# Kernel optimization log

Measured on AMD Instinct MI355X. Metric: run time of the kernel, lower is better.

The kernel has to match this reference:

```python
import jax, jax.numpy as jnp
import numpy as np

# dims
B, SL, RATIO = 2, 2048, 16
SG = SL // RATIO            # 128 global tokens
S = SL + SG                 # 2176 combined sequence
V, D, H, F, L, NC = 32000, 512, 8, 2048, 2, 8
HD = D // H
PAD = 0


def setup_inputs() -> dict:
    key = jax.random.key(0)
    ks = iter(jax.random.split(key, 40))
    def n(shape, s=0.02):
        return jax.random.normal(next(ks), shape, dtype=jnp.float32) * s
    token_ids = jax.random.randint(next(ks), (B, SL), 0, V)
    embed_table = n((V, D), 1.0).at[PAD].set(0.0)  # padding_idx row is zero
    return {
        "token_ids": token_ids,
        "embed_table": embed_table,
        "global_embed": n((D,), 1.0),              # shared learned global token
        "in_proj_w": n((L, 3 * D, D)), "in_proj_b": jnp.zeros((L, 3 * D)),
        "out_w": n((L, D, D)), "out_b": jnp.zeros((L, D)),
        "ln1_g": jnp.ones((L, D)), "ln1_b": jnp.zeros((L, D)),
        "ln2_g": jnp.ones((L, D)), "ln2_b": jnp.zeros((L, D)),
        "ff1_w": n((L, F, D)), "ff1_b": jnp.zeros((L, F)),
        "ff2_w": n((L, D, F)), "ff2_b": jnp.zeros((L, D)),
        "cls_w1": n((D // 2, D)), "cls_w2": n((NC, D // 2)),
    }


def _layernorm(x, g, b, eps=1e-5):
    mu = x.mean(-1, keepdims=True)
    var = ((x - mu) ** 2).mean(-1, keepdims=True)
    return (x - mu) * jax.lax.rsqrt(var + eps) * g + b


def _etc_bias(pad_long, pad_glob):
    # structured local/global mask: l2l block-diagonal by segment, l2g/g2l
    # long<->its own global token, g2g full. All four components enabled.
    seg = jnp.repeat(jnp.arange(SG), RATIO)          # (SL,) segment id per long token
    gid = jnp.arange(SG)
    l2l = seg[:, None] == seg[None, :]               # (SL, SL)
    l2g = seg[:, None] == gid[None, :]               # (SL, SG)
    allowed = jnp.block([[l2l, l2g],
                         [l2g.T, jnp.ones((SG, SG), bool)]])  # (S, S)
    kpad = jnp.concatenate([pad_long, pad_glob], axis=1)       # (B, S)
    ok = allowed[None] & (~kpad)[:, None, :]
    return jnp.where(ok, 0.0, -1e9)[:, None]          # (B, 1, S, S)


def reference(token_ids, embed_table, global_embed, in_proj_w, in_proj_b,
              out_w, out_b, ln1_g, ln1_b, ln2_g, ln2_b,
              ff1_w, ff1_b, ff2_w, ff2_b, cls_w1, cls_w2):
    pad_long = token_ids == PAD                      # (B, SL)
    pad_glob = pad_long.reshape(B, SG, RATIO).all(-1)  # (B, SG)
    x_long = embed_table[token_ids]                  # (B, SL, D)
    x_glob = jnp.broadcast_to(global_embed, (B, SG, D))
    x = jnp.concatenate([x_long, x_glob], axis=1)    # (B, S, D)
    bias = _etc_bias(pad_long, pad_glob)
    scale = 1.0 / np.sqrt(HD)
    for i in range(L):  # post-norm TransformerEncoderLayer, relu FFN, dropout=0
        qkv = x @ in_proj_w[i].T + in_proj_b[i]
        q, k, v = jnp.split(qkv, 3, axis=-1)
        q = q.reshape(B, S, H, HD)
        k = k.reshape(B, S, H, HD)
        v = v.reshape(B, S, H, HD)
        att = jnp.einsum('bqhd,bkhd->bhqk', q, k) * scale + bias
        att = jax.nn.softmax(att, axis=-1)
        o = jnp.einsum('bhqk,bkhd->bqhd', att, v).reshape(B, S, D)
        x = _layernorm(x + o @ out_w[i].T + out_b[i], ln1_g[i], ln1_b[i])
        h = jax.nn.relu(x @ ff1_w[i].T + ff1_b[i])
        x = _layernorm(x + h @ ff2_w[i].T + ff2_b[i], ln2_g[i], ln2_b[i])
    # masked mean-pool over global tokens
    zg = jnp.where(pad_glob[..., None], 0.0, x[:, SL:, :])
    denom = (~pad_glob).sum(axis=1, keepdims=True).astype(zg.dtype)
    z_cls = zg.sum(axis=1) / denom                   # (B, D)
    return jax.nn.relu(z_cls @ cls_w1.T) @ cls_w2.T  # (B, NC)
```

## Files before the change

### kernel.cpp

```cpp
#include <hip/hip_runtime.h>
#include <hip/hip_bf16.h>
#include <stdint.h>


namespace {

constexpr int kB  = 2;
constexpr int kSL = 2048;
constexpr int kSG = 128;
constexpr int kS  = 2176;
constexpr int kD  = 512;
constexpr int kH  = 8;
constexpr int kF  = 2048;
constexpr int kNC = 8;
constexpr int kM  = kB * kS;

typedef __bf16 bf16x8 __attribute__((ext_vector_type(8)));
typedef unsigned short u16x8 __attribute__((ext_vector_type(8)));
typedef float  f32x4  __attribute__((ext_vector_type(4)));
using bf16 = __hip_bfloat16;

__device__ __forceinline__ void gload16(const void* g, void* l) {
  __builtin_amdgcn_global_load_lds(
      (const __attribute__((address_space(1))) void*)g,
      (__attribute__((address_space(3))) void*)l, 16, 0, 0);
}

__device__ __forceinline__ float bfu2f(unsigned short u) {
  return __uint_as_float(((unsigned int)u) << 16);
}

__device__ __forceinline__ int xcd_swz(int i, int T) {
  return (i & 7) * (T >> 3) + (i >> 3);
}

__global__ __launch_bounds__(256) void cvt4_kernel(
    const float* __restrict__ s0, bf16* __restrict__ d0,
    const float* __restrict__ s1, bf16* __restrict__ d1,
    const float* __restrict__ s2, bf16* __restrict__ d2,
    const float* __restrict__ s3, bf16* __restrict__ d3) {
  constexpr int n0 = 2 * 1536 * 512 / 4;
  constexpr int n1 = 2 * 512 * 512 / 4;
  constexpr int n2 = 2 * 2048 * 512 / 4;
  constexpr int n3 = 2 * 512 * 2048 / 4;
  constexpr int total = n0 + n1 + n2 + n3;
  for (int i = blockIdx.x * 256 + threadIdx.x; i < total;
       i += gridDim.x * 256) {
    const float* src;
    bf16* dst;
    int j = i;
    if (j < n0) { src = s0; dst = d0; }
    else if ((j -= n0) < n1) { src = s1; dst = d1; }
    else if ((j -= n1) < n2) { src = s2; dst = d2; }
    else { j -= n2; src = s3; dst = d3; }
    float4 v = ((const float4*)src)[j];
    dst[j * 4 + 0] = __float2bfloat16(v.x);
    dst[j * 4 + 1] = __float2bfloat16(v.y);
    dst[j * 4 + 2] = __float2bfloat16(v.z);
    dst[j * 4 + 3] = __float2bfloat16(v.w);
  }
}

__global__ __launch_bounds__(128) void embed_kernel(
    const int* __restrict__ tok, const float* __restrict__ table,
    const float* __restrict__ gemb, float* __restrict__ x,
    bf16* __restrict__ x_bf, unsigned char* __restrict__ pad_long,
    unsigned char* __restrict__ pad_glob) {
  const int row = blockIdx.x;
  const int t = threadIdx.x;
  if (row == kM) {
    for (int i = t; i < kB * kSG; i += 128) {
      const int b = i >> 7, g = i & 127;
      bool all = true;
      for (int j = 0; j < 16; ++j)
        all = all && (tok[b * kSL + g * 16 + j] == 0);
      pad_glob[i] = all ? 1 : 0;
    }
    return;
  }
  const int b = row / kS, s = row % kS;
  const float* src;
  if (s < kSL) {
    const int tk = tok[b * kSL + s];
    if (t == 0) pad_long[b * kSL + s] = (tk == 0) ? 1 : 0;
    src = table + (size_t)tk * kD;
  } else {
    src = gemb;
  }
  float4 v = *(const float4*)(src + t * 4);
  *(float4*)(x + (size_t)row * kD + t * 4) = v;
  bf16* xb = x_bf + (size_t)row * kD + t * 4;
  xb[0] = __float2bfloat16(v.x);
  xb[1] = __float2bfloat16(v.y);
  xb[2] = __float2bfloat16(v.z);
  xb[3] = __float2bfloat16(v.w);
}

template <int OUT_MODE>
__global__ __launch_bounds__(256) void gemm_bt(
    const bf16* __restrict__ A, const bf16* __restrict__ W,
    const float* __restrict__ bias, void* __restrict__ Cout,
    int M, int N, int K) {
  __shared__ __align__(16) bf16 As[128 * 32];
  __shared__ __align__(16) bf16 Bs[128 * 32];
  const int t = threadIdx.x;
  const int lane = t & 63;
  const int wid = t >> 6;
  const int wm = wid >> 1, wn = wid & 1;
  const int NB = N >> 7;
  const int swz = xcd_swz(blockIdx.x, gridDim.x);
  const int bm = (swz / NB) * 128, bn = (swz % NB) * 128;
  const int srow = t >> 2, scol = (t & 3) * 8;

  f32x4 acc[4][4];
#pragma unroll
  for (int mi = 0; mi < 4; ++mi)
#pragma unroll
    for (int ni = 0; ni < 4; ++ni)
#pragma unroll
      for (int r = 0; r < 4; ++r) acc[mi][ni][r] = 0.f;

  const bf16* a0 = A + (size_t)(bm + srow) * K + scol;
  const bf16* a1 = a0 + (size_t)64 * K;
  const bf16* w0 = W + (size_t)(bn + srow) * K + scol;
  const bf16* w1p = w0 + (size_t)64 * K;

  for (int k0 = 0; k0 < K; k0 += 32) {
    gload16(a0 + k0, &As[t * 8]);
    gload16(a1 + k0, &As[2048 + t * 8]);
    gload16(w0 + k0, &Bs[t * 8]);
    gload16(w1p + k0, &Bs[2048 + t * 8]);
    __syncthreads();
    bf16x8 af[4], wf[4];
#pragma unroll
    for (int mi = 0; mi < 4; ++mi)
      af[mi] = *(const bf16x8*)&As[(wm * 64 + mi * 16 + (lane & 15)) * 32 +
                                   (lane >> 4) * 8];
#pragma unroll
    for (int ni = 0; ni < 4; ++ni)
      wf[ni] = *(const bf16x8*)&Bs[(wn * 64 + ni * 16 + (lane & 15)) * 32 +
                                   (lane >> 4) * 8];
#pragma unroll
    for (int mi = 0; mi < 4; ++mi)
#pragma unroll
      for (int ni = 0; ni < 4; ++ni)
        acc[mi][ni] = __builtin_amdgcn_mfma_f32_16x16x32_bf16(
            af[mi], wf[ni], acc[mi][ni], 0, 0, 0);
    __syncthreads();
  }

  const int lr = (lane >> 4) * 4;
  const int lc = lane & 15;
#pragma unroll
  for (int ni = 0; ni < 4; ++ni) {
    const int col = bn + wn * 64 + ni * 16 + lc;
    const float bv = bias[col];
#pragma unroll
    for (int mi = 0; mi < 4; ++mi) {
#pragma unroll
      for (int r = 0; r < 4; ++r) {
        const int row = bm + wm * 64 + mi * 16 + lr + r;
        float v = acc[mi][ni][r] + bv;
        if (OUT_MODE == 2) v = fmaxf(v, 0.f);
        ((bf16*)Cout)[(size_t)row * N + col] = __float2bfloat16(v);
      }
    }
  }
}

__global__ __launch_bounds__(256) void gemm_res(
    const bf16* __restrict__ A, const bf16* __restrict__ W,
    const float* __restrict__ bias, float* __restrict__ X, int K) {
  __shared__ __align__(16) bf16 As[64 * 32];
  __shared__ __align__(16) bf16 Bs[64 * 32];
  const int t = threadIdx.x;
  const int lane = t & 63;
  const int wid = t >> 6;
  const int wm = wid >> 1, wn = wid & 1;
  const int swz = xcd_swz(blockIdx.x, gridDim.x);
  const int bm = (swz >> 3) * 64, bn = (swz & 7) * 64;
  const int srow = t >> 2, scol = (t & 3) * 8;

  f32x4 acc[2][2];
#pragma unroll
  for (int mi = 0; mi < 2; ++mi)
#pragma unroll
    for (int ni = 0; ni < 2; ++ni)
#pragma unroll
      for (int r = 0; r < 4; ++r) acc[mi][ni][r] = 0.f;

  const bf16* a0 = A + (size_t)(bm + srow) * K + scol;
  const bf16* w0 = W + (size_t)(bn + srow) * K + scol;

  for (int k0 = 0; k0 < K; k0 += 32) {
    gload16(a0 + k0, &As[t * 8]);
    gload16(w0 + k0, &Bs[t * 8]);
    __syncthreads();
    bf16x8 af[2], wf[2];
#pragma unroll
    for (int mi = 0; mi < 2; ++mi)
      af[mi] = *(const bf16x8*)&As[(wm * 32 + mi * 16 + (lane & 15)) * 32 +
                                   (lane >> 4) * 8];
#pragma unroll
    for (int ni = 0; ni < 2; ++ni)
      wf[ni] = *(const bf16x8*)&Bs[(wn * 32 + ni * 16 + (lane & 15)) * 32 +
                                   (lane >> 4) * 8];
#pragma unroll
    for (int mi = 0; mi < 2; ++mi)
#pragma unroll
      for (int ni = 0; ni < 2; ++ni)
        acc[mi][ni] = __builtin_amdgcn_mfma_f32_16x16x32_bf16(
            af[mi], wf[ni], acc[mi][ni], 0, 0, 0);
    __syncthreads();
  }

  const int lr = (lane >> 4) * 4;
  const int lc = lane & 15;
#pragma unroll
  for (int ni = 0; ni < 2; ++ni) {
    const int col = bn + wn * 32 + ni * 16 + lc;
    const float bv = bias[col];
#pragma unroll
    for (int mi = 0; mi < 2; ++mi) {
#pragma unroll
      for (int r = 0; r < 4; ++r) {
        const int row = bm + wm * 32 + mi * 16 + lr + r;
        float* xp = X + (size_t)row * kD + col;
        *xp = *xp + acc[mi][ni][r] + bv;
      }
    }
  }
}

__global__ __launch_bounds__(64) void attn_kernel(
    const bf16* __restrict__ qkv, const unsigned char* __restrict__ padl,
    const unsigned char* __restrict__ padg, bf16* __restrict__ o) {
  __shared__ float lds_buf[17 * 64 * 2];
  const int blk0 = blockIdx.x;
  const int g = blk0 & 127;
  const int h = (blk0 >> 7) & 7;
  const int b = (blk0 >> 10) & 1;
  const int t = threadIdx.x;

  if (blk0 < 2048) {
    float* Ks = lds_buf;
    float* Vs = lds_buf + 17 * 64;
    const int qi = t >> 2, part = t & 3;
    for (int e = t; e < 17 * 64; e += 64) {
      const int j = e >> 6, d = e & 63;
      const size_t row = (j < 16) ? (size_t)(b * kS + g * 16 + j)
                                  : (size_t)(b * kS + kSL + g);
      const bf16* base = qkv + row * (3 * kD) + h * 64 + d;
      Ks[e] = __bfloat162float(base[512]);
      Vs[e] = __bfloat162float(base[1024]);
    }
    __syncthreads();

    float qv[16];
    {
      const bf16* qb = qkv + (size_t)(b * kS + g * 16 + qi) * (3 * kD) +
                       h * 64 + part * 16;
#pragma unroll
      for (int d = 0; d < 16; ++d) qv[d] = __bfloat162float(qb[d]);
    }
    float sc[17];
#pragma unroll
    for (int j = 0; j < 17; ++j) {
      float s = 0.f;
      const float* kb = &Ks[j * 64 + part * 16];
#pragma unroll
      for (int d = 0; d < 16; ++d) s += qv[d] * kb[d];
      s += __shfl_xor(s, 1);
      s += __shfl_xor(s, 2);
      const bool pad = (j < 16) ? (padl[b * kSL + g * 16 + j] != 0)
                                : (padg[b * kSG + g] != 0);
      sc[j] = s * 0.125f + (pad ? -1e9f : 0.f);
    }
    float m = sc[0];
#pragma unroll
    for (int j = 1; j < 17; ++j) m = fmaxf(m, sc[j]);
    float l = 0.f;
#pragma unroll
    for (int j = 0; j < 17; ++j) {
      sc[j] = __expf(sc[j] - m);
      l += sc[j];
    }
    const float inv = 1.f / l;
    float ov[16];
#pragma unroll
    for (int d = 0; d < 16; ++d) ov[d] = 0.f;
#pragma unroll
    for (int j = 0; j < 17; ++j) {
      const float* vb = &Vs[j * 64 + part * 16];
#pragma unroll
      for (int d = 0; d < 16; ++d) ov[d] += sc[j] * vb[d];
    }
    bf16* ob = o + (size_t)(b * kS + g * 16 + qi) * kD + h * 64 + part * 16;
#pragma unroll
    for (int d = 0; d < 16; ++d) ob[d] = __float2bfloat16(ov[d] * inv);
  } else {
    float* q_lds = lds_buf;
    float* p_lds = lds_buf + 64;
    const size_t qrow = (size_t)(b * kS + kSL + g);
    const unsigned short* qkv_u = (const unsigned short*)qkv;
    q_lds[t] = bfu2f(qkv_u[qrow * 1536 + h * 64 + t]);
    __syncthreads();

    float sc[3];
#pragma unroll
    for (int c = 0; c < 3; ++c) {
      const int j = t + c * 64;
      float s = -3.0e38f;
      if (j < 144) {
        const size_t krow = (j < 16) ? (size_t)(b * kS + g * 16 + j)
                                     : (size_t)(b * kS + kSL + (j - 16));
        const u16x8* kb = (const u16x8*)(qkv_u + krow * 1536 + 512 + h * 64);
        float acc = 0.f;
#pragma unroll
        for (int d0 = 0; d0 < 8; ++d0) {
          u16x8 kv = kb[d0];
#pragma unroll
          for (int u = 0; u < 8; ++u) acc += q_lds[d0 * 8 + u] * bfu2f(kv[u]);
        }
        const bool pad = (j < 16) ? (padl[b * kSL + g * 16 + j] != 0)
                                  : (padg[b * kSG + (j - 16)] != 0);
        s = acc * 0.125f + (pad ? -1e9f : 0.f);
      }
      sc[c] = s;
    }
    float m = fmaxf(fmaxf(sc[0], sc[1]), sc[2]);
#pragma unroll
    for (int off = 1; off < 64; off <<= 1) m = fmaxf(m, __shfl_xor(m, off));
    float lsum = 0.f;
#pragma unroll
    for (int c = 0; c < 3; ++c) {
      const int j = t + c * 64;
      if (j < 144) {
        const float p = __expf(sc[c] - m);
        p_lds[j] = p;
        lsum += p;
      }
    }
#pragma unroll
    for (int off = 1; off < 64; off <<= 1) lsum += __shfl_xor(lsum, off);
    __syncthreads();
    const float inv = 1.f / lsum;

    float ov = 0.f;
#pragma unroll 8
    for (int j = 0; j < 144; ++j) {
      const size_t vrow = (j < 16) ? (size_t)(b * kS + g * 16 + j)
                                   : (size_t)(b * kS + kSL + (j - 16));
      ov += p_lds[j] * bfu2f(qkv_u[vrow * 1536 + 1024 + h * 64 + t]);
    }
    o[qrow * kD + h * 64 + t] = __float2bfloat16(ov * inv);
  }
}

__global__ __launch_bounds__(256) void ln_kernel(
    float* __restrict__ x, const float* __restrict__ gamma,
    const float* __restrict__ beta, bf16* __restrict__ x_bf) {
  const int row = blockIdx.x, t = threadIdx.x;
  const size_t base = (size_t)row * kD;
  float v0 = x[base + t];
  float v1 = x[base + t + 256];
  float s = v0 + v1, q = v0 * v0 + v1 * v1;
#pragma unroll
  for (int off = 32; off > 0; off >>= 1) {
    s += __shfl_down(s, off);
    q += __shfl_down(q, off);
  }
  __shared__ float rs[4], rq[4];
  const int wid = t >> 6;
  if ((t & 63) == 0) { rs[wid] = s; rq[wid] = q; }
  __syncthreads();
  const float S = rs[0] + rs[1] + rs[2] + rs[3];
  const float Q = rq[0] + rq[1] + rq[2] + rq[3];
  const float mean = S * (1.f / kD);
  const float var = Q * (1.f / kD) - mean * mean;
  const float inv = rsqrtf(var + 1e-5f);
  const float y0 = (v0 - mean) * inv * gamma[t] + beta[t];
  const float y1 = (v1 - mean) * inv * gamma[t + 256] + beta[t + 256];
  x[base + t] = y0;
  x[base + t + 256] = y1;
  x_bf[base + t] = __float2bfloat16(y0);
  x_bf[base + t + 256] = __float2bfloat16(y1);
}

__global__ __launch_bounds__(256) void pool_kernel(
    const float* __restrict__ x, const unsigned char* __restrict__ padg,
    float* __restrict__ z) {
  const int b = blockIdx.x >> 5;
  const int d0 = (blockIdx.x & 31) * 16;
  const int gg = threadIdx.x >> 4, dl = threadIdx.x & 15;
  float acc = 0.f;
  int cnt = 0;
#pragma unroll
  for (int k = 0; k < 8; ++k) {
    const int g = k * 16 + gg;
    if (padg[b * kSG + g] == 0) {
      acc += x[(size_t)(b * kS + kSL + g) * kD + d0 + dl];
      ++cnt;
    }
  }
  __shared__ float red[256];
  __shared__ int redc[256];
  red[threadIdx.x] = acc;
  redc[threadIdx.x] = cnt;
  __syncthreads();
  for (int s = 8; s > 0; s >>= 1) {
    if (gg < s) {
      red[gg * 16 + dl] += red[(gg + s) * 16 + dl];
      redc[gg * 16 + dl] += redc[(gg + s) * 16 + dl];
    }
    __syncthreads();
  }
  if (gg == 0) z[b * kD + d0 + dl] = red[dl] / (float)redc[dl];
}

__global__ __launch_bounds__(256) void cls1_kernel(
    const float* __restrict__ z, const float* __restrict__ w1,
    float* __restrict__ h1) {
  const int wv = (blockIdx.x * 256 + threadIdx.x) >> 6;
  const int lane = threadIdx.x & 63;
  const int b = wv >> 8, t = wv & 255;
  const float4* zp = (const float4*)(z + b * kD);
  const float4* wp = (const float4*)(w1 + (size_t)t * kD);
  float4 a0 = zp[lane * 2], a1 = zp[lane * 2 + 1];
  float4 b0 = wp[lane * 2], b1 = wp[lane * 2 + 1];
  float acc = a0.x * b0.x + a0.y * b0.y + a0.z * b0.z + a0.w * b0.w +
              a1.x * b1.x + a1.y * b1.y + a1.z * b1.z + a1.w * b1.w;
#pragma unroll
  for (int off = 32; off > 0; off >>= 1) acc += __shfl_down(acc, off);
  if (lane == 0) h1[wv] = fmaxf(acc, 0.f);
}

__global__ __launch_bounds__(64) void cls2_kernel(
    const float* __restrict__ h1, const float* __restrict__ w2,
    float* __restrict__ out) {
  const int wv = blockIdx.x;
  const int lane = threadIdx.x;
  const int b = wv >> 3, c = wv & 7;
  float4 h4 = ((const float4*)(h1 + b * 256))[lane];
  float4 w4 = ((const float4*)(w2 + c * 256))[lane];
  float acc = h4.x * w4.x + h4.y * w4.y + h4.z * w4.z + h4.w * w4.w;
#pragma unroll
  for (int off = 32; off > 0; off >>= 1) acc += __shfl_down(acc, off);
  if (lane == 0) out[wv] = acc;
}

}

extern "C" void kernel_launch(void* const* d_in, const int* in_sizes, int n_in,
                              void* d_out, int out_size, void* d_ws,
                              size_t ws_size, hipStream_t stream) {
  (void)in_sizes; (void)n_in; (void)out_size; (void)ws_size;
  const int*   token_ids    = (const int*)d_in[0];
  const float* embed_table  = (const float*)d_in[1];
  const float* global_embed = (const float*)d_in[2];
  const float* in_proj_w    = (const float*)d_in[3];
  const float* in_proj_b    = (const float*)d_in[4];
  const float* out_w        = (const float*)d_in[5];
  const float* out_b        = (const float*)d_in[6];
  const float* ln1_g        = (const float*)d_in[7];
  const float* ln1_b        = (const float*)d_in[8];
  const float* ln2_g        = (const float*)d_in[9];
  const float* ln2_b        = (const float*)d_in[10];
  const float* ff1_w        = (const float*)d_in[11];
  const float* ff1_b        = (const float*)d_in[12];
  const float* ff2_w        = (const float*)d_in[13];
  const float* ff2_b        = (const float*)d_in[14];
  const float* cls_w1       = (const float*)d_in[15];
  const float* cls_w2       = (const float*)d_in[16];
  float* out = (float*)d_out;

  char* ws = (char*)d_ws;
  size_t off = 0;
  auto alloc = [&](size_t bytes) -> void* {
    void* p = ws + off;
    off += (bytes + 255) & ~(size_t)255;
    return p;
  };
  float* x_f   = (float*)alloc((size_t)kM * kD * 4);
  bf16*  x_b   = (bf16*)alloc((size_t)kM * kD * 2);
  bf16*  qkv_b = (bf16*)alloc((size_t)kM * 3 * kD * 2);
  bf16*  o_b   = (bf16*)alloc((size_t)kM * kD * 2);
  bf16*  h_b   = (bf16*)alloc((size_t)kM * kF * 2);
  bf16*  wqkv  = (bf16*)alloc((size_t)2 * 1536 * 512 * 2);
  bf16*  wout  = (bf16*)alloc((size_t)2 * 512 * 512 * 2);
  bf16*  wff1  = (bf16*)alloc((size_t)2 * 2048 * 512 * 2);
  bf16*  wff2  = (bf16*)alloc((size_t)2 * 512 * 2048 * 2);
  unsigned char* padl = (unsigned char*)alloc(kB * kSL);
  unsigned char* padg = (unsigned char*)alloc(kB * kSG);
  float* z_f   = (float*)alloc((size_t)kB * kD * 4);
  float* h1_f  = (float*)alloc((size_t)kB * 256 * 4);

  cvt4_kernel<<<2048, 256, 0, stream>>>(in_proj_w, wqkv, out_w, wout,
                                        ff1_w, wff1, ff2_w, wff2);

  embed_kernel<<<kM + 1, 128, 0, stream>>>(token_ids, embed_table,
                                           global_embed, x_f, x_b, padl, padg);

  for (int l = 0; l < 2; ++l) {
    gemm_bt<1><<<(1536 / 128) * (kM / 128), 256, 0, stream>>>(
        x_b, wqkv + (size_t)l * 1536 * 512, in_proj_b + l * 1536, qkv_b,
        kM, 1536, 512);
    attn_kernel<<<2 * kB * kH * kSG, 64, 0, stream>>>(qkv_b, padl, padg, o_b);
    gemm_res<<<8 * (kM / 64), 256, 0, stream>>>(
        o_b, wout + (size_t)l * 512 * 512, out_b + l * 512, x_f, 512);
    ln_kernel<<<kM, 256, 0, stream>>>(x_f, ln1_g + l * 512, ln1_b + l * 512,
                                      x_b);
    gemm_bt<2><<<(2048 / 128) * (kM / 128), 256, 0, stream>>>(
        x_b, wff1 + (size_t)l * 2048 * 512, ff1_b + l * 2048, h_b,
        kM, 2048, 512);
    gemm_res<<<8 * (kM / 64), 256, 0, stream>>>(
        h_b, wff2 + (size_t)l * 512 * 2048, ff2_b + l * 512, x_f, 2048);
    ln_kernel<<<kM, 256, 0, stream>>>(x_f, ln2_g + l * 512, ln2_b + l * 512,
                                      x_b);
  }

  pool_kernel<<<kB * 32, 256, 0, stream>>>(x_f, padg, z_f);
  cls1_kernel<<<128, 256, 0, stream>>>(z_f, cls_w1, h1_f);
  cls2_kernel<<<16, 64, 0, stream>>>(h1_f, cls_w2, out);
}
```

Before: 375.3 us.

## Triple-buffer LDS tiles in GEMM kernels with async global-to-LDS prefetch

Both the projection GEMM and the residual GEMM now keep three LDS stages and issue global_load_lds for tiles two iterations ahead. Explicit vmcnt waits plus a raw s_barrier replace the load-then-syncthreads pattern, so memory latency overlaps with MFMA work. This triples LDS use per block, which may lower occupancy. The hand-written waitcnt counts must match exactly how many loads are in flight.

```diff
diff --git a/kernel.cpp b/kernel.cpp
--- a/kernel.cpp
+++ b/kernel.cpp
@@ -101,8 +101,8 @@
     const bf16* __restrict__ A, const bf16* __restrict__ W,
     const float* __restrict__ bias, void* __restrict__ Cout,
     int M, int N, int K) {
-  __shared__ __align__(16) bf16 As[128 * 32];
-  __shared__ __align__(16) bf16 Bs[128 * 32];
+  __shared__ __align__(16) bf16 As[3][128 * 32];
+  __shared__ __align__(16) bf16 Bs[3][128 * 32];
   const int t = threadIdx.x;
   const int lane = t & 63;
   const int wid = t >> 6;
@@ -125,28 +125,45 @@
   const bf16* w0 = W + (size_t)(bn + srow) * K + scol;
   const bf16* w1p = w0 + (size_t)64 * K;
 
-  for (int k0 = 0; k0 < K; k0 += 32) {
-    gload16(a0 + k0, &As[t * 8]);
-    gload16(a1 + k0, &As[2048 + t * 8]);
-    gload16(w0 + k0, &Bs[t * 8]);
-    gload16(w1p + k0, &Bs[2048 + t * 8]);
-    __syncthreads();
+  auto stage = [&](int kt, int buf) {
+    const int k0 = kt * 32;
+    gload16(a0 + k0, &As[buf][t * 8]);
+    gload16(a1 + k0, &As[buf][2048 + t * 8]);
+    gload16(w0 + k0, &Bs[buf][t * 8]);
+    gload16(w1p + k0, &Bs[buf][2048 + t * 8]);
+  };
+
+  const int nt = K >> 5;
+  stage(0, 0);
+  stage(1, 1);
+  for (int kt = 0; kt < nt; ++kt) {
+    const int cur = kt % 3;
+    const int nxt = kt + 2;
+    if (nxt < nt) {
+      stage(nxt, nxt % 3);
+      asm volatile("s_waitcnt vmcnt(8)" ::: "memory");
+    } else if (kt + 1 < nt) {
+      asm volatile("s_waitcnt vmcnt(4)" ::: "memory");
+    } else {
+      asm volatile("s_waitcnt vmcnt(0)" ::: "memory");
+    }
+    __builtin_amdgcn_s_barrier();
     bf16x8 af[4], wf[4];
 #pragma unroll
     for (int mi = 0; mi < 4; ++mi)
-      af[mi] = *(const bf16x8*)&As[(wm * 64 + mi * 16 + (lane & 15)) * 32 +
-                                   (lane >> 4) * 8];
+      af[mi] = *(const bf16x8*)&As[cur][(wm * 64 + mi * 16 + (lane & 15)) * 32 +
+                                        (lane >> 4) * 8];
 #pragma unroll
     for (int ni = 0; ni < 4; ++ni)
-      wf[ni] = *(const bf16x8*)&Bs[(wn * 64 + ni * 16 + (lane & 15)) * 32 +
-                                   (lane >> 4) * 8];
+      wf[ni] = *(const bf16x8*)&Bs[cur][(wn * 64 + ni * 16 + (lane & 15)) * 32 +
+                                        (lane >> 4) * 8];
 #pragma unroll
     for (int mi = 0; mi < 4; ++mi)
 #pragma unroll
       for (int ni = 0; ni < 4; ++ni)
         acc[mi][ni] = __builtin_amdgcn_mfma_f32_16x16x32_bf16(
             af[mi], wf[ni], acc[mi][ni], 0, 0, 0);
-    __syncthreads();
+    __builtin_amdgcn_s_barrier();
   }
 
   const int lr = (lane >> 4) * 4;
@@ -171,8 +188,8 @@
 __global__ __launch_bounds__(256) void gemm_res(
     const bf16* __restrict__ A, const bf16* __restrict__ W,
     const float* __restrict__ bias, float* __restrict__ X, int K) {
-  __shared__ __align__(16) bf16 As[64 * 32];
-  __shared__ __align__(16) bf16 Bs[64 * 32];
+  __shared__ __align__(16) bf16 As[3][64 * 32];
+  __shared__ __align__(16) bf16 Bs[3][64 * 32];
   const int t = threadIdx.x;
   const int lane = t & 63;
   const int wid = t >> 6;
@@ -192,26 +209,43 @@
   const bf16* a0 = A + (size_t)(bm + srow) * K + scol;
   const bf16* w0 = W + (size_t)(bn + srow) * K + scol;
 
-  for (int k0 = 0; k0 < K; k0 += 32) {
-    gload16(a0 + k0, &As[t * 8]);
-    gload16(w0 + k0, &Bs[t * 8]);
-    __syncthreads();
+  auto stage = [&](int kt, int buf) {
+    const int k0 = kt * 32;
+    gload16(a0 + k0, &As[buf][t * 8]);
+    gload16(w0 + k0, &Bs[buf][t * 8]);
+  };
+
+  const int nt = K >> 5;
+  stage(0, 0);
+  stage(1, 1);
+  for (int kt = 0; kt < nt; ++kt) {
+    const int cur = kt % 3;
+    const int nxt = kt + 2;
+    if (nxt < nt) {
+      stage(nxt, nxt % 3);
+      asm volatile("s_waitcnt vmcnt(4)" ::: "memory");
+    } else if (kt + 1 < nt) {
+      asm volatile("s_waitcnt vmcnt(2)" ::: "memory");
+    } else {
+      asm volatile("s_waitcnt vmcnt(0)" ::: "memory");
+    }
+    __builtin_amdgcn_s_barrier();
     bf16x8 af[2], wf[2];
 #pragma unroll
     for (int mi = 0; mi < 2; ++mi)
-      af[mi] = *(const bf16x8*)&As[(wm * 32 + mi * 16 + (lane & 15)) * 32 +
-                                   (lane >> 4) * 8];
+      af[mi] = *(const bf16x8*)&As[cur][(wm * 32 + mi * 16 + (lane & 15)) * 32 +
+                                        (lane >> 4) * 8];
 #pragma unroll
     for (int ni = 0; ni < 2; ++ni)
-      wf[ni] = *(const bf16x8*)&Bs[(wn * 32 + ni * 16 + (lane & 15)) * 32 +
-                                   (lane >> 4) * 8];
+      wf[ni] = *(const bf16x8*)&Bs[cur][(wn * 32 + ni * 16 + (lane & 15)) * 32 +
+                                        (lane >> 4) * 8];
 #pragma unroll
     for (int mi = 0; mi < 2; ++mi)
 #pragma unroll
       for (int ni = 0; ni < 2; ++ni)
         acc[mi][ni] = __builtin_amdgcn_mfma_f32_16x16x32_bf16(
             af[mi], wf[ni], acc[mi][ni], 0, 0, 0);
-    __syncthreads();
+    __builtin_amdgcn_s_barrier();
   }
 
   const int lr = (lane >> 4) * 4;
```

After: 369.8 us. About the same (-1.5%).
